# Performance work log

Measured on AMD Instinct MI355X. Metric: run time of the kernel, lower is better.

Reference implementation:

```python
import jax, jax.numpy as jnp
import numpy as np

PROTO_M = 0.99  # cfg.proto_m
EPS = 1e-12     # F.normalize eps

N, D, C, Q = 256, 128, 1000, 262144


def setup_inputs() -> dict:
    key = jax.random.key(0)
    ks = jax.random.split(key, 8)
    return {
        "q_x": jax.random.normal(ks[0], (N, D), jnp.float32),
        "k_x": jax.random.normal(ks[1], (N, D), jnp.float32),
        "output_x": jax.random.normal(ks[2], (N, C), jnp.float32),
        "queue": jax.random.normal(ks[3], (Q, D), jnp.float32),
        "prototypes": jax.random.normal(ks[4], (C, D), jnp.float32),
        "isID": jnp.zeros((Q,), jnp.float32),
        "Y": jax.random.randint(ks[5], (N,), 0, C),
        "queue_Y": jax.random.randint(ks[6], (Q,), 0, C),
        "ptr": 0,
    }


def _ema_prototypes(prototypes, feats, labels, m):
    """Vectorized equivalent of the sequential per-sample EMA loop:
        for feat, label in zip(feats, labels):
            prototypes[label] = prototypes[label]*m + (1-m)*feat
    Closed form (order-exact, handles duplicate labels):
        proto[c] = m^cnt_c * proto[c] + (1-m) * sum_i m^(cnt_c-1-rank_i) * feat_i
    """
    n = feats.shape[0]
    c = prototypes.shape[0]
    same = labels[:, None] == labels[None, :]                    # [N,N]
    rank = jnp.sum(jnp.tril(same, -1), axis=1).astype(feats.dtype)  # prior same-label occurrences
    cnt = jax.ops.segment_sum(jnp.ones((n,), feats.dtype), labels, num_segments=c)  # [C]
    w = (1.0 - m) * m ** (cnt[labels] - 1.0 - rank)              # [N] per-sample weight
    contrib = jax.ops.segment_sum(w[:, None] * feats, labels, num_segments=c)       # [C,D]
    new = prototypes * (m ** cnt)[:, None] + contrib
    norm = jnp.maximum(jnp.linalg.norm(new, axis=1, keepdims=True), EPS)
    return new / norm  # F.normalize(prototypes, p=2, dim=1)


def reference(q_x, k_x, output_x, queue, prototypes, isID, Y, queue_Y, ptr):
    n = q_x.shape[0]
    q_len = queue.shape[0]
    # prototype EMA scatter + renormalize (buffer update, no grad in torch)
    new_protos = _ema_prototypes(prototypes, q_x, Y, PROTO_M)
    # moco_queue features/targets (queue is detached in torch)
    features = jnp.concatenate([q_x, k_x, queue], axis=0)          # [2N+Q, D]
    targets = jnp.concatenate([Y, Y, queue_Y], axis=0)             # [2N+Q]
    # _dequeue_and_enqueue2 with isid = ones(N)
    new_queue = jax.lax.dynamic_update_slice(queue, k_x, (ptr, 0))
    new_queue_Y = jax.lax.dynamic_update_slice(queue_Y, Y, (ptr,))
    new_isID = jax.lax.dynamic_update_slice(isID, jnp.ones((n,), isID.dtype), (ptr,))
    new_ptr = (ptr + n) % q_len
    return (output_x, features, targets, new_protos, new_queue, new_queue_Y, new_isID, new_ptr)
```

## Files before the change

### kernel.cpp

```cpp
#include <hip/hip_runtime.h>
#include <math.h>

constexpr int  Nn = 256;
constexpr int  Dd = 128;
constexpr int  Cc = 1000;
constexpr int  Qq = 262144;
constexpr float PROTO_M = 0.99f;

typedef float vf4 __attribute__((ext_vector_type(4)));
typedef int   vi4 __attribute__((ext_vector_type(4)));

constexpr long SEG_OUTX  = (long)Nn * Cc / 4;
constexpr long SEG_QX    = (long)Nn * Dd / 4;
constexpr long SEG_QUEUE = (long)Qq * Dd / 4;
constexpr long SEG_TGT   = (long)(2 * Nn + Qq) / 4;
constexpr long SEG_QY    = (long)Qq / 4;

constexpr long OFF_OUTX = 0;
constexpr long OFF_FEAT = (long)Nn * Cc;
constexpr long OFF_TGT  = OFF_FEAT + (long)(2 * Nn + Qq) * Dd;
constexpr long OFF_PROT = OFF_TGT + (2 * Nn + Qq);
constexpr long OFF_NQ   = OFF_PROT + (long)Cc * Dd;
constexpr long OFF_NQY  = OFF_NQ + (long)Qq * Dd;
constexpr long OFF_ISID = OFF_NQY + Qq;
constexpr long OFF_PTR  = OFF_ISID + Qq;

constexpr int PROTO_BLOCKS = Cc / 2;
constexpr int COPY_BLOCKS  = 4096;

__global__ __launch_bounds__(256) void mega_kernel(
    const vf4* __restrict__ q_x4, const vf4* __restrict__ k_x4,
    const vf4* __restrict__ output_x4, const vf4* __restrict__ queue4,
    const float* __restrict__ protos, const vf4* __restrict__ isID4,
    const int* __restrict__ Y, const int* __restrict__ queue_Y,
    const int* __restrict__ ptr_p, float* __restrict__ out)
{
    if (blockIdx.x < PROTO_BLOCKS) {
        const float* q_x = (const float*)q_x4;
        const int grp = threadIdx.x >> 7;
        const int c   = blockIdx.x * 2 + grp;
        const int d   = threadIdx.x & 127;
        float p = protos[(long)c * Dd + d];
        const float m = PROTO_M, om = 1.0f - PROTO_M;
        for (int i = 0; i < Nn; ++i) {
            int y = Y[i];
            if (y == c) p = m * p + om * q_x[(long)i * Dd + d];
        }
        float s = p * p;
        #pragma unroll
        for (int off = 32; off >= 1; off >>= 1) s += __shfl_xor(s, off);
        __shared__ float ws[4];
        if ((threadIdx.x & 63) == 0) ws[threadIdx.x >> 6] = s;
        __syncthreads();
        float norm = fmaxf(sqrtf(ws[2 * grp] + ws[2 * grp + 1]), 1e-12f);
        out[OFF_PROT + (long)c * Dd + d] = p / norm;
        return;
    }

    const long total = SEG_OUTX + 2 * SEG_QX + SEG_QUEUE + SEG_TGT + 2 * SEG_QY + 1;
    vf4* out4 = (vf4*)out;
    const vi4* Y4  = (const vi4*)Y;
    const vi4* qY4 = (const vi4*)queue_Y;

    const int ptr_raw = *ptr_p;
    const int ptr = min(max(ptr_raw, 0), Qq - Nn);

    const long stride = (long)COPY_BLOCKS * blockDim.x;
    for (long v = (long)(blockIdx.x - PROTO_BLOCKS) * blockDim.x + threadIdx.x;
         v < total; v += stride) {
        long r = v;
        if (r < SEG_OUTX) {
            vf4 t = __builtin_nontemporal_load(output_x4 + r);
            __builtin_nontemporal_store(t, out4 + OFF_OUTX / 4 + r);
            continue;
        }
        r -= SEG_OUTX;
        if (r < SEG_QX) {
            vf4 t = q_x4[r];
            __builtin_nontemporal_store(t, out4 + OFF_FEAT / 4 + r);
            continue;
        }
        r -= SEG_QX;
        if (r < SEG_QX) {
            vf4 t = k_x4[r];
            __builtin_nontemporal_store(t, out4 + OFF_FEAT / 4 + SEG_QX + r);
            continue;
        }
        r -= SEG_QX;
        if (r < SEG_QUEUE) {
            vf4 qv = __builtin_nontemporal_load(queue4 + r);
            __builtin_nontemporal_store(qv, out4 + OFF_FEAT / 4 + 2 * SEG_QX + r);
            int row = (int)(r >> 5);
            vf4 nq = qv;
            if (row >= ptr && row < ptr + Nn)
                nq = k_x4[((long)(row - ptr) << 5) + (r & 31)];
            __builtin_nontemporal_store(nq, out4 + OFF_NQ / 4 + r);
            continue;
        }
        r -= SEG_QUEUE;
        if (r < SEG_TGT) {
            vi4 t;
            if (r < Nn / 4)            t = Y4[r];
            else if (r < 2 * Nn / 4)   t = Y4[r - Nn / 4];
            else                       t = qY4[r - 2 * Nn / 4];
            vf4 o = { (float)t.x, (float)t.y, (float)t.z, (float)t.w };
            __builtin_nontemporal_store(o, out4 + OFF_TGT / 4 + r);
            continue;
        }
        r -= SEG_TGT;
        if (r < SEG_QY) {
            vi4 t = qY4[r];
            vf4 o = { (float)t.x, (float)t.y, (float)t.z, (float)t.w };
            long e0 = r << 2;
            if (e0 + 3 >= ptr && e0 < (long)ptr + Nn) {
                #pragma unroll
                for (int c2 = 0; c2 < 4; ++c2) {
                    long e = e0 + c2;
                    if (e >= ptr && e < (long)ptr + Nn) o[c2] = (float)Y[e - ptr];
                }
            }
            __builtin_nontemporal_store(o, out4 + OFF_NQY / 4 + r);
            continue;
        }
        r -= SEG_QY;
        if (r < SEG_QY) {
            vf4 o = __builtin_nontemporal_load(isID4 + r);
            long e0 = r << 2;
            if (e0 + 3 >= ptr && e0 < (long)ptr + Nn) {
                #pragma unroll
                for (int c2 = 0; c2 < 4; ++c2) {
                    long e = e0 + c2;
                    if (e >= ptr && e < (long)ptr + Nn) o[c2] = 1.0f;
                }
            }
            __builtin_nontemporal_store(o, out4 + OFF_ISID / 4 + r);
            continue;
        }
        out[OFF_PTR] = (float)((ptr_raw + Nn) % Qq);
    }
}

extern "C" void kernel_launch(void* const* d_in, const int* in_sizes, int n_in,
                              void* d_out, int out_size, void* d_ws, size_t ws_size,
                              hipStream_t stream)
{
    const float* q_x      = (const float*)d_in[0];
    const float* k_x      = (const float*)d_in[1];
    const float* output_x = (const float*)d_in[2];
    const float* queue    = (const float*)d_in[3];
    const float* protos   = (const float*)d_in[4];
    const float* isID     = (const float*)d_in[5];
    const int*   Y        = (const int*)d_in[6];
    const int*   queue_Y  = (const int*)d_in[7];
    const int*   ptr_p    = (const int*)d_in[8];
    float* out = (float*)d_out;

    hipLaunchKernelGGL(mega_kernel, dim3(PROTO_BLOCKS + COPY_BLOCKS), dim3(256), 0, stream,
                       (const vf4*)q_x, (const vf4*)k_x,
                       (const vf4*)output_x, (const vf4*)queue,
                       protos, (const vf4*)isID, Y, queue_Y, ptr_p, out);
}
```

Baseline: 81.44 us.

## Split queue copy into dedicated contiguous-chunk blocks, reorder block roles

The large queue copy (and new_queue write) now gets its own set of blocks, each handling a contiguous 2560-vector chunk with two loads issued per iteration, which removes the per-element segment dispatch from the hot path. The remaining small segments go to a separate grid-stride group of 512 blocks, and the prototype EMA blocks move to the end of the grid. This aims to improve memory-level parallelism and cut branch overhead on the dominant copy. In exchange the grid grows to roughly 4200 blocks, and the serial 256-step prototype loop is now scheduled last, where it could sit in the tail.

```diff
diff --git a/kernel.cpp b/kernel.cpp
--- a/kernel.cpp
+++ b/kernel.cpp
@@ -25,8 +25,11 @@
 constexpr long OFF_ISID = OFF_NQY + Qq;
 constexpr long OFF_PTR  = OFF_ISID + Qq;
 
-constexpr int PROTO_BLOCKS = Cc / 2;
-constexpr int COPY_BLOCKS  = 4096;
+constexpr long CH       = 2560;
+constexpr int  QBLOCKS  = (int)((SEG_QUEUE + CH - 1) / CH);
+constexpr int  OBLOCKS  = 512;
+constexpr int  PBLOCKS  = Cc / 2;
+constexpr long OTHER_TOTAL = SEG_OUTX + 2 * SEG_QX + SEG_TGT + 2 * SEG_QY + 1;
 
 __global__ __launch_bounds__(256) void mega_kernel(
     const vf4* __restrict__ q_x4, const vf4* __restrict__ k_x4,
@@ -35,11 +38,109 @@
     const int* __restrict__ Y, const int* __restrict__ queue_Y,
     const int* __restrict__ ptr_p, float* __restrict__ out)
 {
-    if (blockIdx.x < PROTO_BLOCKS) {
+    vf4* out4 = (vf4*)out;
+    const int bid = blockIdx.x;
+    const int t   = threadIdx.x;
+
+    const int ptr_raw = *ptr_p;
+    const int ptr = min(max(ptr_raw, 0), Qq - Nn);
+
+    if (bid < QBLOCKS) {
+        vf4* __restrict__ feat4 = out4 + OFF_FEAT / 4 + 2 * SEG_QX;
+        vf4* __restrict__ nq4   = out4 + OFF_NQ / 4;
+        const long s = (long)bid * CH;
+        const long e = min(s + CH, SEG_QUEUE);
+        for (long i = s + t; i < e; i += 512) {
+            const long j = i + 256;
+            vf4 a = __builtin_nontemporal_load(queue4 + i);
+            vf4 b = __builtin_nontemporal_load(queue4 + j);
+            __builtin_nontemporal_store(a, feat4 + i);
+            __builtin_nontemporal_store(b, feat4 + j);
+            const int rowa = (int)(i >> 5);
+            const int rowb = (int)(j >> 5);
+            vf4 na = a, nb = b;
+            if (rowa >= ptr && rowa < ptr + Nn)
+                na = k_x4[((long)(rowa - ptr) << 5) + (i & 31)];
+            if (rowb >= ptr && rowb < ptr + Nn)
+                nb = k_x4[((long)(rowb - ptr) << 5) + (j & 31)];
+            __builtin_nontemporal_store(na, nq4 + i);
+            __builtin_nontemporal_store(nb, nq4 + j);
+        }
+        return;
+    }
+
+    if (bid < QBLOCKS + OBLOCKS) {
+        const vi4* Y4  = (const vi4*)Y;
+        const vi4* qY4 = (const vi4*)queue_Y;
+        const long stride = (long)OBLOCKS * 256;
+        for (long v = (long)(bid - QBLOCKS) * 256 + t; v < OTHER_TOTAL; v += stride) {
+            long r = v;
+            if (r < SEG_OUTX) {
+                vf4 x = __builtin_nontemporal_load(output_x4 + r);
+                __builtin_nontemporal_store(x, out4 + OFF_OUTX / 4 + r);
+                continue;
+            }
+            r -= SEG_OUTX;
+            if (r < SEG_QX) {
+                vf4 x = q_x4[r];
+                __builtin_nontemporal_store(x, out4 + OFF_FEAT / 4 + r);
+                continue;
+            }
+            r -= SEG_QX;
+            if (r < SEG_QX) {
+                vf4 x = k_x4[r];
+                __builtin_nontemporal_store(x, out4 + OFF_FEAT / 4 + SEG_QX + r);
+                continue;
+            }
+            r -= SEG_QX;
+            if (r < SEG_TGT) {
+                vi4 x;
+                if (r < Nn / 4)          x = Y4[r];
+                else if (r < 2 * Nn / 4) x = Y4[r - Nn / 4];
+                else                     x = qY4[r - 2 * Nn / 4];
+                vf4 o = { (float)x.x, (float)x.y, (float)x.z, (float)x.w };
+                __builtin_nontemporal_store(o, out4 + OFF_TGT / 4 + r);
+                continue;
+            }
+            r -= SEG_TGT;
+            if (r < SEG_QY) {
+                vi4 x = qY4[r];
+                vf4 o = { (float)x.x, (float)x.y, (float)x.z, (float)x.w };
+                long e0 = r << 2;
+                if (e0 + 3 >= ptr && e0 < (long)ptr + Nn) {
+                    #pragma unroll
+                    for (int c2 = 0; c2 < 4; ++c2) {
+                        long e = e0 + c2;
+                        if (e >= ptr && e < (long)ptr + Nn) o[c2] = (float)Y[e - ptr];
+                    }
+                }
+                __builtin_nontemporal_store(o, out4 + OFF_NQY / 4 + r);
+                continue;
+            }
+            r -= SEG_QY;
+            if (r < SEG_QY) {
+                vf4 o = __builtin_nontemporal_load(isID4 + r);
+                long e0 = r << 2;
+                if (e0 + 3 >= ptr && e0 < (long)ptr + Nn) {
+                    #pragma unroll
+                    for (int c2 = 0; c2 < 4; ++c2) {
+                        long e = e0 + c2;
+                        if (e >= ptr && e < (long)ptr + Nn) o[c2] = 1.0f;
+                    }
+                }
+                __builtin_nontemporal_store(o, out4 + OFF_ISID / 4 + r);
+                continue;
+            }
+            out[OFF_PTR] = (float)((ptr_raw + Nn) % Qq);
+        }
+        return;
+    }
+
+    {
         const float* q_x = (const float*)q_x4;
-        const int grp = threadIdx.x >> 7;
-        const int c   = blockIdx.x * 2 + grp;
-        const int d   = threadIdx.x & 127;
+        const int grp = t >> 7;
+        const int c   = (bid - QBLOCKS - OBLOCKS) * 2 + grp;
+        const int d   = t & 127;
         float p = protos[(long)c * Dd + d];
         const float m = PROTO_M, om = 1.0f - PROTO_M;
         for (int i = 0; i < Nn; ++i) {
@@ -50,93 +151,10 @@
         #pragma unroll
         for (int off = 32; off >= 1; off >>= 1) s += __shfl_xor(s, off);
         __shared__ float ws[4];
-        if ((threadIdx.x & 63) == 0) ws[threadIdx.x >> 6] = s;
+        if ((t & 63) == 0) ws[t >> 6] = s;
         __syncthreads();
         float norm = fmaxf(sqrtf(ws[2 * grp] + ws[2 * grp + 1]), 1e-12f);
         out[OFF_PROT + (long)c * Dd + d] = p / norm;
-        return;
-    }
-
-    const long total = SEG_OUTX + 2 * SEG_QX + SEG_QUEUE + SEG_TGT + 2 * SEG_QY + 1;
-    vf4* out4 = (vf4*)out;
-    const vi4* Y4  = (const vi4*)Y;
-    const vi4* qY4 = (const vi4*)queue_Y;
-
-    const int ptr_raw = *ptr_p;
-    const int ptr = min(max(ptr_raw, 0), Qq - Nn);
-
-    const long stride = (long)COPY_BLOCKS * blockDim.x;
-    for (long v = (long)(blockIdx.x - PROTO_BLOCKS) * blockDim.x + threadIdx.x;
-         v < total; v += stride) {
-        long r = v;
-        if (r < SEG_OUTX) {
-            vf4 t = __builtin_nontemporal_load(output_x4 + r);
-            __builtin_nontemporal_store(t, out4 + OFF_OUTX / 4 + r);
-            continue;
-        }
-        r -= SEG_OUTX;
-        if (r < SEG_QX) {
-            vf4 t = q_x4[r];
-            __builtin_nontemporal_store(t, out4 + OFF_FEAT / 4 + r);
-            continue;
-        }
-        r -= SEG_QX;
-        if (r < SEG_QX) {
-            vf4 t = k_x4[r];
-            __builtin_nontemporal_store(t, out4 + OFF_FEAT / 4 + SEG_QX + r);
-            continue;
-        }
-        r -= SEG_QX;
-        if (r < SEG_QUEUE) {
-            vf4 qv = __builtin_nontemporal_load(queue4 + r);
-            __builtin_nontemporal_store(qv, out4 + OFF_FEAT / 4 + 2 * SEG_QX + r);
-            int row = (int)(r >> 5);
-            vf4 nq = qv;
-            if (row >= ptr && row < ptr + Nn)
-                nq = k_x4[((long)(row - ptr) << 5) + (r & 31)];
-            __builtin_nontemporal_store(nq, out4 + OFF_NQ / 4 + r);
-            continue;
-        }
-        r -= SEG_QUEUE;
-        if (r < SEG_TGT) {
-            vi4 t;
-            if (r < Nn / 4)            t = Y4[r];
-            else if (r < 2 * Nn / 4)   t = Y4[r - Nn / 4];
-            else                       t = qY4[r - 2 * Nn / 4];
-            vf4 o = { (float)t.x, (float)t.y, (float)t.z, (float)t.w };
-            __builtin_nontemporal_store(o, out4 + OFF_TGT / 4 + r);
-            continue;
-        }
-        r -= SEG_TGT;
-        if (r < SEG_QY) {
-            vi4 t = qY4[r];
-            vf4 o = { (float)t.x, (float)t.y, (float)t.z, (float)t.w };
-            long e0 = r << 2;
-            if (e0 + 3 >= ptr && e0 < (long)ptr + Nn) {
-                #pragma unroll
-                for (int c2 = 0; c2 < 4; ++c2) {
-                    long e = e0 + c2;
-                    if (e >= ptr && e < (long)ptr + Nn) o[c2] = (float)Y[e - ptr];
-                }
-            }
-            __builtin_nontemporal_store(o, out4 + OFF_NQY / 4 + r);
-            continue;
-        }
-        r -= SEG_QY;
-        if (r < SEG_QY) {
-            vf4 o = __builtin_nontemporal_load(isID4 + r);
-            long e0 = r << 2;
-            if (e0 + 3 >= ptr && e0 < (long)ptr + Nn) {
-                #pragma unroll
-                for (int c2 = 0; c2 < 4; ++c2) {
-                    long e = e0 + c2;
-                    if (e >= ptr && e < (long)ptr + Nn) o[c2] = 1.0f;
-                }
-            }
-            __builtin_nontemporal_store(o, out4 + OFF_ISID / 4 + r);
-            continue;
-        }
-        out[OFF_PTR] = (float)((ptr_raw + Nn) % Qq);
     }
 }
 
@@ -155,7 +173,7 @@
     const int*   ptr_p    = (const int*)d_in[8];
     float* out = (float*)d_out;
 
-    hipLaunchKernelGGL(mega_kernel, dim3(PROTO_BLOCKS + COPY_BLOCKS), dim3(256), 0, stream,
+    hipLaunchKernelGGL(mega_kernel, dim3(QBLOCKS + OBLOCKS + PBLOCKS), dim3(256), 0, stream,
                        (const vf4*)q_x, (const vf4*)k_x,
                        (const vf4*)output_x, (const vf4*)queue,
                        protos, (const vf4*)isID, Y, queue_Y, ptr_p, out);
```

Result: slower. 88.83 us (+9.1%).
